# Kernel optimization log

Hardware: AMD Instinct MI355X
Metric: run time of the kernel (lower is better)

## Reference

```python
import jax, jax.numpy as jnp
import numpy as np

A = -0.75  # torch bicubic cubic-convolution coefficient

def _cubic_k(t):
    at = jnp.abs(t)
    return jnp.where(at <= 1, (A + 2) * at**3 - (A + 3) * at**2 + 1,
           jnp.where(at < 2, A * at**3 - 5 * A * at**2 + 8 * A * at - 4 * A, 0.0))

def _resize_last(x, out_size):
    # bicubic, align_corners=True, along last axis
    in_size = x.shape[-1]
    pos = jnp.arange(out_size, dtype=x.dtype) * ((in_size - 1) / (out_size - 1))
    i0 = jnp.floor(pos).astype(jnp.int32)
    frac = pos - i0
    offs = jnp.arange(-1, 3, dtype=jnp.int32)                    # 4 taps
    idx = jnp.clip(i0[None] + offs[:, None], 0, in_size - 1)     # [4, out]
    w = _cubic_k(frac[None] - offs[:, None].astype(x.dtype))     # [4, out]
    g = x[..., idx]                                              # [..., 4, out]
    return jnp.einsum('...ko,ko->...o', g, w)

def bicubic(x, H, W):
    x = _resize_last(x, W)
    x = jnp.swapaxes(_resize_last(jnp.swapaxes(x, -1, -2), H), -1, -2)
    return x

def conv(x, w, b):
    y = jax.lax.conv_general_dilated(x, w, (1, 1), 'SAME',
                                     dimension_numbers=('NCHW', 'OIHW', 'NCHW'))
    return y + b[None, :, None, None]

def pool(x):
    return jax.lax.reduce_window(x, -jnp.inf, jax.lax.max, (1, 1, 2, 2), (1, 1, 2, 2), 'VALID')

def extract(x, ws, bs):
    # feat1: vgg19 features[:2]
    x1 = jax.nn.relu(conv(x, ws[0], bs[0]))
    # feat2: vgg19 features[2:18]
    h = jax.nn.relu(conv(x1, ws[1], bs[1])); h = pool(h)
    h = jax.nn.relu(conv(h, ws[2], bs[2]))
    h = jax.nn.relu(conv(h, ws[3], bs[3])); h = pool(h)
    for i in range(4, 8):
        h = jax.nn.relu(conv(h, ws[i], bs[i]))
    h = bicubic(h, x1.shape[-2], x1.shape[-1])
    return jnp.concatenate([x1, h], axis=1)  # [B, 320, H, W]

def normalizer(f1, f2):
    B, C = f1.shape[:2]
    a = f1.reshape(B, C, -1)
    b = f2.reshape(B, C, -1)
    xc = jnp.concatenate([a, b], axis=-1)
    mean = xc.mean(-1, keepdims=True)
    std = xc.mean(-1, keepdims=True)  # faithful to original source bug: std = mean
    a = (a - mean) / (std + 1e-8)
    b = (b - mean) / (std + 1e-8)
    return a.reshape(f1.shape), b.reshape(f2.shape)

_CHANS = [(3, 64), (64, 64), (64, 128), (128, 128), (128, 256), (256, 256), (256, 256), (256, 256)]

def setup_inputs() -> dict:
    key = jax.random.key(0)
    ks = jax.random.split(key, 20)
    inp = {}
    for i, (ci, co) in enumerate(_CHANS):
        inp[f'w{i}'] = jax.random.normal(ks[i], (co, ci, 3, 3), jnp.float32) * np.sqrt(2.0 / (ci * 9))
        inp[f'b{i}'] = jnp.zeros((co,), jnp.float32)
    inp['x_ref'] = jax.random.normal(ks[16], (2, 3, 96, 96), jnp.float32)
    inp['x_template'] = jax.random.normal(ks[17], (2, 3, 48, 48), jnp.float32)
    inp['coef_ref'] = jnp.float32(1.0)
    inp['coef_tmp'] = jnp.float32(1.0)
    return inp

def reference(x_ref, x_template, coef_ref, coef_tmp,
              w0, b0, w1, b1, w2, b2, w3, b3, w4, b4, w5, b5, w6, b6, w7, b7):
    ws = [w0, w1, w2, w3, w4, w5, w6, w7]
    bs = [b0, b1, b2, b3, b4, b5, b6, b7]
    fref = extract(x_ref, ws, bs)
    ftem = extract(x_template, ws, bs)
    fref, ftem = normalizer(fref, ftem)
    B, C, m, n = fref.shape
    _, _, p, q = ftem.shape
    dist = jnp.einsum('bcmn,bcpq->bmnpq', fref, ftem).reshape(B, m * n, p * q)
    conf_ref = jax.nn.softmax(coef_ref * dist, axis=-2)
    conf_tmp = jax.nn.softmax(coef_tmp * dist, axis=-1)
    confidence = jnp.sqrt(conf_ref * conf_tmp)
    vals, _ = jax.lax.top_k(confidence, 10)
    values = vals.mean(-1, keepdims=True).reshape(B, m, n, 1)
    return values
```

## Files before the change

### kernel.cpp

```cpp
#include <hip/hip_runtime.h>
#include <math.h>

#define CK_A (-0.75f)

typedef __attribute__((ext_vector_type(8))) short bf16x8;
typedef __attribute__((ext_vector_type(4))) float f32x4;

struct CImg { const void* in; void* out; int H, W, tiles; long inBS, outBS, sStride; };

__device__ __forceinline__ float cubicw(float t){
  float at = fabsf(t);
  float at2 = at*at, at3 = at2*at;
  if (at <= 1.f) return (CK_A+2.f)*at3 - (CK_A+3.f)*at2 + 1.f;
  if (at < 2.f)  return CK_A*at3 - 5.f*CK_A*at2 + 8.f*CK_A*at - 4.f*CK_A;
  return 0.f;
}

__device__ __forceinline__ unsigned short f2bf_rne(float f){
  unsigned int u = __float_as_uint(f);
  unsigned int r = (u + 0x7fffu + ((u>>16)&1u)) >> 16;
  return (unsigned short)r;
}
__device__ __forceinline__ float bf2f(unsigned short h){
  return __uint_as_float(((unsigned int)h)<<16);
}
__device__ __forceinline__ unsigned pack_bf(float v){
  unsigned short h = f2bf_rne(v);
  unsigned short l = f2bf_rne(v - bf2f(h));
  return ((unsigned)h<<16) | (unsigned)l;
}
__device__ __forceinline__ float unpack_bf(unsigned p){
  return bf2f((unsigned short)(p>>16)) + bf2f((unsigned short)(p&0xffffu));
}

__device__ __forceinline__ void merge_ms(float& m, float& s, float m2, float s2){
  float M = fmaxf(m, m2);
  s = s*__expf(m - M) + s2*__expf(m2 - M);
  m = M;
}

#define MFB(a,b,c) __builtin_amdgcn_mfma_f32_16x16x32_bf16(a,b,c,0,0,0)

typedef const __attribute__((address_space(1))) unsigned int* gp1_t;
typedef __attribute__((address_space(3))) unsigned int* lp3_t;
__device__ __forceinline__ void dma16(const void* g, void* l){
  __builtin_amdgcn_global_load_lds((gp1_t)g, (lp3_t)l, 16, 0, 0);
}

__global__ __launch_bounds__(256) void conv0_d(CImg A, CImg B,
    const float* __restrict__ w, const float* __restrict__ bias,
    unsigned* __restrict__ pOutA, unsigned* __restrict__ pOutB){
  bool isA = (int)blockIdx.x < A.tiles;
  const float* in = (const float*)(isA ? A.in : B.in);
  float* out = (float*)(isA ? A.out : B.out);
  unsigned* pout = isA ? pOutA : pOutB;
  int H = isA ? A.H : B.H, W = isA ? A.W : B.W;
  long inBS = isA ? A.inBS : B.inBS, outBS = isA ? A.outBS : B.outBS;
  int tile = isA ? blockIdx.x : blockIdx.x - A.tiles;
  int tilesX = (W + 15) >> 4;
  int tx0 = (tile % tilesX) << 4, ty0 = (tile / tilesX) << 4;
  int cob = blockIdx.y * 4;
  int b = blockIdx.z;
  int lx = threadIdx.x & 15, ly = threadIdx.x >> 4;
  __shared__ float tile_s[3][18][20];
  float acc[4] = {0.f,0.f,0.f,0.f};
  const float* inb = in + (long)b*inBS;
  int ox = tx0+lx, oy = ty0+ly;
  int HW = H*W;

  for (int idx = threadIdx.x; idx < 3*324; idx += 256){
    int cl = idx/324, rem = idx - cl*324;
    int r = rem/18, c = rem - r*18;
    int gy = ty0 + r - 1, gx = tx0 + c - 1;
    const float* ic = inb + (long)cl*HW;
    tile_s[cl][r][c] = (gy>=0 && gy<H && gx>=0 && gx<W) ? ic[(long)gy*W+gx] : 0.f;
  }
  __syncthreads();
  #pragma unroll
  for (int cl=0; cl<3; cl++){
    float t00=tile_s[cl][ly+0][lx+0], t01=tile_s[cl][ly+0][lx+1], t02=tile_s[cl][ly+0][lx+2];
    float t10=tile_s[cl][ly+1][lx+0], t11=tile_s[cl][ly+1][lx+1], t12=tile_s[cl][ly+1][lx+2];
    float t20=tile_s[cl][ly+2][lx+0], t21=tile_s[cl][ly+2][lx+1], t22=tile_s[cl][ly+2][lx+2];
    #pragma unroll
    for (int j=0;j<4;j++){
      const float* wp = w + ((long)(cob+j)*3 + cl)*9;
      float a = acc[j];
      a = fmaf(t00, wp[0], a); a = fmaf(t01, wp[1], a); a = fmaf(t02, wp[2], a);
      a = fmaf(t10, wp[3], a); a = fmaf(t11, wp[4], a); a = fmaf(t12, wp[5], a);
      a = fmaf(t20, wp[6], a); a = fmaf(t21, wp[7], a); a = fmaf(t22, wp[8], a);
      acc[j] = a;
    }
  }
  if (ox < W && oy < H){
    #pragma unroll
    for (int j=0;j<4;j++){
      float v = fmaxf(acc[j] + bias[cob+j], 0.f);
      long pix = (long)(cob+j)*HW + (long)oy*W + ox;
      out[(long)b*outBS + pix] = v;
      pout[(long)b*64*HW + pix] = pack_bf(v);
    }
  }
}

__global__ void prep_w_all(const float* __restrict__ w1, const float* __restrict__ w2,
                           const float* __restrict__ w3, const float* __restrict__ w4,
                           const float* __restrict__ w5, const float* __restrict__ w6,
                           const float* __restrict__ w7, unsigned short* __restrict__ wp){
  const int ciT[7] = {64,64,128,128,256,256,256};
  const int coT[7] = {64,128,128,256,256,256,256};
  int l = blockIdx.y;
  const float* w = l==0?w1: l==1?w2: l==2?w3: l==3?w4: l==4?w5: l==5?w6: w7;
  long offv = 0;
  for (int i=0;i<7;i++){ if (i<l) offv += 9L*ciT[i]*coT[i]*2; }
  long total = 9L*ciT[l]*coT[l]*2;
  long e = (long)blockIdx.x*256 + threadIdx.x;
  if (e >= total) return;
  int CI = ciT[l], CO = coT[l];
  int j = (int)(e & 7);
  int lane = (int)((e>>3) & 63);
  int h = (int)((e>>9) & 1);
  long rem = e >> 10;
  int G = CO >> 4, KC = CI >> 5;
  int g = (int)(rem % G); long q = rem / G;
  int kc = (int)(q % KC); int o = (int)(q / KC);
  int co = (g<<4) + (lane & 15);
  int ci = (kc<<5) + ((lane>>4)<<3) + j;
  float v = w[((long)co*CI + ci)*9 + o];
  unsigned short hi = f2bf_rne(v);
  wp[offv + e] = (h==0) ? hi : f2bf_rne(v - bf2f(hi));
}

union AB { bf16x8 v; uint4 u; };

__global__ __launch_bounds__(256) void conv_mfma_d(
    CImg A, CImg B, const unsigned short* __restrict__ Wp,
    const float* __restrict__ bias, int CI, int CO, int nci, int S)
{
  bool isA = (int)blockIdx.x < A.tiles;
  const unsigned* in = (const unsigned*)(isA ? A.in : B.in);
  void* outv = isA ? A.out : B.out;
  int H = isA ? A.H : B.H, W = isA ? A.W : B.W;
  long inBS = isA ? A.inBS : B.inBS, outBS = isA ? A.outBS : B.outBS;
  long sStride = isA ? A.sStride : B.sStride;
  int tile = isA ? blockIdx.x : blockIdx.x - A.tiles;

  int HW = H*W;
  int tilesX = (W+7)>>3;
  int tx0 = (tile % tilesX)<<3, ty0 = (tile / tilesX)<<3;
  int cobase = blockIdx.y << 6;
  int s = blockIdx.z % S, b = blockIdx.z / S;
  int tid = threadIdx.x, lane = tid & 63, wid = tid>>6;
  int wm = wid>>1, wn = wid&1;
  int KC = CI>>5, G = CO>>4;
  __shared__ __align__(16) unsigned short Bth[4000];
  __shared__ __align__(16) unsigned short Btl[4000];
  const unsigned* inb = in + (long)b*inBS;

  int sofs[13]; int sla[13];
  #pragma unroll
  for (int i=0;i<13;i++){
    int e = tid + i*256;
    int cidx = e / 100, pix = e - cidx*100;
    int hy = pix/10, hx = pix - hy*10;
    int gy = ty0 - 1 + hy, gx = tx0 - 1 + hx;
    bool v = (gy>=0) && (gy<H) && (gx>=0) && (gx<W);
    sofs[i] = v ? (cidx*HW + gy*W + gx) : -1;
    sla[i] = pix*40 + cidx;
  }

  int n15 = lane & 15;
  int klane8 = (lane>>4)<<3;
  int p0 = wn*32 + n15;
  int base0 = ((p0>>3)*10 + (p0&7))*40 + klane8;
  int p1 = p0 + 16;
  int base1 = ((p1>>3)*10 + (p1&7))*40 + klane8;
  int g0 = (cobase>>4) + wm*2;

  f32x4 acc[2][2];
  #pragma unroll
  for (int i=0;i<2;i++)
    #pragma unroll
    for (int j=0;j<2;j++) acc[i][j] = (f32x4){0.f,0.f,0.f,0.f};

  int nkc = nci >> 5;
  for (int kk=0; kk<nkc; kk++){
    int ci0 = s*nci + (kk<<5);
    __syncthreads();
    #pragma unroll
    for (int i=0;i<12;i++){
      unsigned p = (sofs[i] >= 0) ? inb[(long)ci0*HW + sofs[i]] : 0u;
      Bth[sla[i]] = (unsigned short)(p>>16);
      Btl[sla[i]] = (unsigned short)(p & 0xffffu);
    }
    if (tid < 128){
      unsigned p = (sofs[12] >= 0) ? inb[(long)ci0*HW + sofs[12]] : 0u;
      Bth[sla[12]] = (unsigned short)(p>>16);
      Btl[sla[12]] = (unsigned short)(p & 0xffffu);
    }
    __syncthreads();
    int kc = ci0 >> 5;
    const unsigned short* wpb = Wp + (long)kc*G*1024 + (long)lane*8;
    #pragma unroll
    for (int o=0;o<9;o++){
      const int dy = o/3, dx = o - dy*3;
      const int sh = (dy*10+dx)*40;
      const unsigned short* wo = wpb + (long)o*KC*G*1024;
      AB a0h,a0l,a1h,a1l, b0h,b0l,b1h,b1l;
      a0h.u = *(const uint4*)(wo + (long)g0*1024);
      a0l.u = *(const uint4*)(wo + (long)g0*1024 + 512);
      a1h.u = *(const uint4*)(wo + (long)(g0+1)*1024);
      a1l.u = *(const uint4*)(wo + (long)(g0+1)*1024 + 512);
      b0h.v = *(const bf16x8*)&Bth[base0 + sh];
      b0l.v = *(const bf16x8*)&Btl[base0 + sh];
      b1h.v = *(const bf16x8*)&Bth[base1 + sh];
      b1l.v = *(const bf16x8*)&Btl[base1 + sh];
      acc[0][0] = MFB(a0h.v, b0l.v, acc[0][0]);
      acc[0][0] = MFB(a0l.v, b0h.v, acc[0][0]);
      acc[0][0] = MFB(a0h.v, b0h.v, acc[0][0]);
      acc[0][1] = MFB(a0h.v, b1l.v, acc[0][1]);
      acc[0][1] = MFB(a0l.v, b1h.v, acc[0][1]);
      acc[0][1] = MFB(a0h.v, b1h.v, acc[0][1]);
      acc[1][0] = MFB(a1h.v, b0l.v, acc[1][0]);
      acc[1][0] = MFB(a1l.v, b0h.v, acc[1][0]);
      acc[1][0] = MFB(a1h.v, b0h.v, acc[1][0]);
      acc[1][1] = MFB(a1h.v, b1l.v, acc[1][1]);
      acc[1][1] = MFB(a1l.v, b1h.v, acc[1][1]);
      acc[1][1] = MFB(a1h.v, b1h.v, acc[1][1]);
    }
  }

  #pragma unroll
  for (int ng=0; ng<2; ng++){
    int p = wn*32 + ng*16 + n15;
    int gy = ty0 + (p>>3), gx = tx0 + (p&7);
    bool ok = (gy<H) && (gx<W);
    #pragma unroll
    for (int mg=0; mg<2; mg++){
      #pragma unroll
      for (int r=0;r<4;r++){
        if (ok){
          int co = cobase + wm*32 + mg*16 + ((lane>>4)<<2) + r;
          long idx = (long)co*HW + (long)gy*W + gx;
          float v = acc[mg][ng][r];
          if (bias){
            unsigned* outp = (unsigned*)outv + (long)b*outBS;
            outp[idx] = pack_bf(fmaxf(v + bias[co], 0.f));
          } else {
            float* outp = (float*)outv + (long)s*sStride + (long)b*outBS;
            outp[idx] = v;
          }
        }
      }
    }
  }
}

__global__ void reduce_d(const float* __restrict__ pA, const float* __restrict__ pB,
                         const float* __restrict__ bias,
                         unsigned* __restrict__ oA, unsigned* __restrict__ oB,
                         int S, long sStrA, long sStrB, int CO, int HWa, int HWb,
                         long oBSa, long oBSb){
  int img = blockIdx.y;
  const float* part = img ? pB : pA;
  unsigned* out = img ? oB : oA;
  int HW = img ? HWb : HWa;
  long sStride = img ? sStrB : sStrA;
  long outBS = img ? oBSb : oBSa;
  long tot = 2L*CO*HW;
  long e = (long)blockIdx.x*256 + threadIdx.x;
  if (e >= tot) return;
  long b = e / ((long)CO*HW);
  long r = e - b*(long)CO*HW;
  float v = 0.f;
  for (int s=0;s<S;s++) v += part[(long)s*sStride + e];
  int co = (int)(r / HW);
  out[b*outBS + r] = pack_bf(fmaxf(v + bias[co], 0.f));
}

__global__ void maxpool2_d(const unsigned* __restrict__ inA, unsigned* __restrict__ outA, long NCa, int HiA, int WiA,
                           const unsigned* __restrict__ inB, unsigned* __restrict__ outB, long NCb, int HiB, int WiB){
  const unsigned* in = blockIdx.y ? inB : inA;
  unsigned* out = blockIdx.y ? outB : outA;
  long NC = blockIdx.y ? NCb : NCa;
  int Hi = blockIdx.y ? HiB : HiA, Wi = blockIdx.y ? WiB : WiA;
  int Ho = Hi>>1, Wo = Wi>>1;
  long total = NC * Ho * Wo;
  long idx = (long)blockIdx.x*256 + threadIdx.x;
  if (idx >= total) return;
  int x = (int)(idx % Wo); long t = idx / Wo; int y = (int)(t % Ho); long nc = t / Ho;
  const unsigned* p = in + (nc*Hi + 2*y)*(long)Wi + 2*x;
  unsigned c0=p[0], c1=p[1], c2=p[Wi], c3=p[Wi+1];
  float v0=unpack_bf(c0), v1=unpack_bf(c1), v2=unpack_bf(c2), v3=unpack_bf(c3);
  unsigned best=c0; float bv=v0;
  if (v1>bv){bv=v1;best=c1;}
  if (v2>bv){bv=v2;best=c2;}
  if (v3>bv){bv=v3;best=c3;}
  out[idx] = best;
}

__global__ __launch_bounds__(256) void bicubic_d(
    const unsigned* __restrict__ inA, float* __restrict__ outA,
    const unsigned* __restrict__ inB, float* __restrict__ outB){
  int c = blockIdx.x;
  int img = blockIdx.y >> 1, b = blockIdx.y & 1;
  const unsigned* in = img ? inB : inA;
  float* out = img ? outB : outA;
  int Hin = img ? 12 : 24, Win = Hin, Hout = img ? 48 : 96, Wout = Hout;
  long inBS = img ? 256L*144 : 256L*576;
  long outBS = img ? 320L*2304 : 320L*9216;
  __shared__ float s[576];
  const unsigned* ip = in + (long)b*inBS + (long)c*Hin*Win;
  float* op = out + (long)b*outBS + (long)c*Hout*Wout;
  int n = Hin*Win;
  for (int i = threadIdx.x; i < n; i += 256) s[i] = unpack_bf(ip[i]);
  __syncthreads();
  float scy = (float)((double)(Hin-1)/(double)(Hout-1));
  float scx = scy;
  int total = Hout*Wout;
  for (int idx = threadIdx.x; idx < total; idx += 256){
    int ox = idx % Wout, oy = idx / Wout;
    float py = oy * scy, px = ox * scx;
    float iy0f = floorf(py), ix0f = floorf(px);
    int iy0 = (int)iy0f, ix0 = (int)ix0f;
    float fy = py - iy0f, fx = px - ix0f;
    float wy[4], wx[4]; int xs[4], ys[4];
    #pragma unroll
    for (int t=0;t<4;t++){
      wy[t] = cubicw(fy - (float)(t-1));
      wx[t] = cubicw(fx - (float)(t-1));
      ys[t] = min(max(iy0 + t - 1, 0), Hin-1);
      xs[t] = min(max(ix0 + t - 1, 0), Win-1);
    }
    float acc = 0.f;
    #pragma unroll
    for (int i=0;i<4;i++){
      const float* row = &s[ys[i]*Win];
      float rs = wx[0]*row[xs[0]] + wx[1]*row[xs[1]] + wx[2]*row[xs[2]] + wx[3]*row[xs[3]];
      acc = fmaf(wy[i], rs, acc);
    }
    op[idx] = acc;
  }
}

__global__ __launch_bounds__(256) void mean_k(const float* __restrict__ fR, const float* __restrict__ fT, float* __restrict__ mean){
  int c = blockIdx.x % 320, b = blockIdx.x / 320;
  const float* a = fR + ((long)b*320+c)*9216L;
  const float* t = fT + ((long)b*320+c)*2304L;
  float s = 0.f;
  for (int i=threadIdx.x;i<9216;i+=256) s += a[i];
  for (int i=threadIdx.x;i<2304;i+=256) s += t[i];
  __shared__ float sm[4];
  for (int o=32;o;o>>=1) s += __shfl_down(s,o);
  int lane = threadIdx.x & 63, wv = threadIdx.x >> 6;
  if (lane==0) sm[wv] = s;
  __syncthreads();
  if (threadIdx.x==0) mean[b*320+c] = (sm[0]+sm[1]+sm[2]+sm[3]) * (1.f/11520.f);
}

__global__ __launch_bounds__(256) void split_bf16_d(const float* __restrict__ fR, const float* __restrict__ fT,
    const float* __restrict__ mean,
    unsigned short* __restrict__ AhR, unsigned short* __restrict__ AlR,
    unsigned short* __restrict__ BhT, unsigned short* __restrict__ BlT){
  bool isR = blockIdx.x < 288;
  const float* feat = isR ? fR : fT;
  unsigned short* oh = isR ? AhR : BhT;
  unsigned short* ol = isR ? AlR : BlT;
  int P = isR ? 9216 : 2304;
  int m0 = (isR ? blockIdx.x : blockIdx.x - 288) * 32;
  int b = blockIdx.y;
  __shared__ unsigned int t[32][321];
  int ml = threadIdx.x & 31, kq = threadIdx.x >> 5;
  const float* fp = feat + (long)b*320*P + m0 + ml;
  for (int k = kq*40; k < kq*40+40; k++){
    float mu = mean[b*320+k];
    float v = (fp[(long)k*P] - mu) / (mu + 1e-8f);
    t[ml][k] = pack_bf(v);
  }
  __syncthreads();
  long base = ((long)b*P + m0)*320;
  for (int idx = threadIdx.x; idx < 32*320; idx += 256){
    int m = idx/320, k = idx - m*320;
    unsigned int p = t[m][k];
    oh[base + (long)m*320 + k] = (unsigned short)(p>>16);
    ol[base + (long)m*320 + k] = (unsigned short)(p & 0xffffu);
  }
}

__global__ __launch_bounds__(256) void gemm_mfma(
    const unsigned short* __restrict__ Ah, const unsigned short* __restrict__ Al,
    const unsigned short* __restrict__ Bh, const unsigned short* __restrict__ Bl,
    float* __restrict__ D, const float* __restrict__ coefr,
    float* __restrict__ pm, float* __restrict__ ps){
  const int N = 2304, K = 320;
  int flat = (int)blockIdx.y * 18 + (int)blockIdx.x;
  int nf = (flat & 7) * 162 + (flat >> 3);
  int mb = nf / 18, nb = nf - mb*18;
  int n0 = nb*128, m0 = mb*128;
  __shared__ __align__(16) unsigned short SF[16384];
  int tid = threadIdx.x, lane = tid & 63, wid = tid >> 6;
  int wm = wid >> 1, wn = wid & 1;
  int n15 = lane & 15, q = lane >> 4;
  f32x4 acc[4][4];
  #pragma unroll
  for (int i=0;i<4;i++)
    #pragma unroll
    for (int j=0;j<4;j++) acc[i][j] = (f32x4){0.f,0.f,0.f,0.f};

  const unsigned short* srcB[8];
  #pragma unroll
  for (int i=0;i<8;i++){
    int li = i*256 + tid;
    int rem = li & 1023;
    int row = rem >> 3, sg = rem & 7;
    int seg = sg ^ (row & 7);
    if (li < 1024) srcB[i] = ((seg<4) ? Ah : Al) + (long)(m0+row)*K + (seg&3)*8;
    else           srcB[i] = ((seg<4) ? Bh : Bl) + (long)(n0+row)*K + (seg&3)*8;
  }

  int aH[4], aL[4], bH[4], bL[4];
  #pragma unroll
  for (int g=0; g<4; g++){
    int ra = wm*64 + g*16 + n15;
    int rb = wn*64 + g*16 + n15;
    aH[g] = ra*64 + (( q   ) ^ (ra&7))*8;
    aL[g] = ra*64 + ((q+4) ^ (ra&7))*8;
    bH[g] = 8192 + rb*64 + (( q   ) ^ (rb&7))*8;
    bL[g] = 8192 + rb*64 + ((q+4) ^ (rb&7))*8;
  }

  for (int k0=0; k0<K; k0+=32){
    __syncthreads();
    #pragma unroll
    for (int i=0;i<8;i++){
      dma16(srcB[i] + k0, (void*)&SF[((i<<8) + (wid<<6))<<3]);
    }
    __syncthreads();

    AB af[2][4], bf[2][4];
    #pragma unroll
    for (int g=0; g<4; g++){
      af[0][g].v = *(const bf16x8*)&SF[aH[g]];
      af[1][g].v = *(const bf16x8*)&SF[aL[g]];
      bf[0][g].v = *(const bf16x8*)&SF[bH[g]];
      bf[1][g].v = *(const bf16x8*)&SF[bL[g]];
    }
    #pragma unroll
    for (int mg=0; mg<4; mg++)
      #pragma unroll
      for (int ng=0; ng<4; ng++){
        acc[mg][ng] = MFB(af[0][mg].v, bf[1][ng].v, acc[mg][ng]);
        acc[mg][ng] = MFB(af[1][mg].v, bf[0][ng].v, acc[mg][ng]);
        acc[mg][ng] = MFB(af[0][mg].v, bf[0][ng].v, acc[mg][ng]);
      }
  }
  __syncthreads();

  #pragma unroll
  for (int mg=0; mg<4; mg++)
    #pragma unroll
    for (int ng=0; ng<4; ng++){
      int col = n0 + wn*64 + ng*16 + n15;
      #pragma unroll
      for (int r=0;r<4;r++){
        int rowv = m0 + wm*64 + mg*16 + q*4 + r;
        __builtin_nontemporal_store(acc[mg][ng][r], &D[(long)rowv*N + col]);
      }
    }

  float cr = *coefr;
  float* red = (float*)&SF[0];
  float pmv[4], psv[4];
  #pragma unroll
  for (int ng=0; ng<4; ng++){
    float m = -INFINITY;
    #pragma unroll
    for (int mg=0; mg<4; mg++)
      #pragma unroll
      for (int r=0;r<4;r++) m = fmaxf(m, cr*acc[mg][ng][r]);
    float s = 0.f;
    #pragma unroll
    for (int mg=0; mg<4; mg++)
      #pragma unroll
      for (int r=0;r<4;r++) s += __expf(cr*acc[mg][ng][r] - m);
    #pragma unroll
    for (int o=16;o<64;o<<=1){
      float m2 = __shfl_xor(m,o), s2 = __shfl_xor(s,o);
      merge_ms(m,s,m2,s2);
    }
    pmv[ng]=m; psv[ng]=s;
  }
  if (q==0){
    #pragma unroll
    for (int ng=0; ng<4; ng++){
      int cl = wn*64 + ng*16 + lane;
      red[wm*128 + cl] = pmv[ng];
      red[256 + wm*128 + cl] = psv[ng];
    }
  }
  __syncthreads();
  if (wm==0 && q==0){
    #pragma unroll
    for (int ng=0; ng<4; ng++){
      int cl = wn*64 + ng*16 + lane;
      float m = pmv[ng], s = psv[ng];
      merge_ms(m, s, red[128+cl], red[384+cl]);
      pm[(long)mb*2304 + n0 + cl] = m;
      ps[(long)mb*2304 + n0 + cl] = s;
    }
  }
}

__global__ void colstat_merge(const float* __restrict__ pm, const float* __restrict__ ps,
                              float* __restrict__ qcol){
  int idx = blockIdx.x*256 + threadIdx.x;
  if (idx >= 2304) return;
  float m=-INFINITY, s=0.f;
  for (int k=0;k<72;k++) merge_ms(m, s, pm[(long)k*2304+idx], ps[(long)k*2304+idx]);
  qcol[idx] = 0.5f*m + 0.5f*__logf(s);
}

__global__ __launch_bounds__(256) void conf_topk_f(const float* __restrict__ D,
    const float* __restrict__ coefr, const float* __restrict__ coeft,
    const float* __restrict__ qcol, float* __restrict__ outp){
  int m = blockIdx.x;
  const float* drow = D + (long)m*2304;
  int tid = threadIdx.x, lane = tid & 63, wv = tid >> 6;
  float ct = *coeft, cr = *coefr;
  float v[9], tv[9];
  #pragma unroll
  for (int i=0;i<9;i++){ v[i] = __builtin_nontemporal_load(&drow[tid + i*256]); tv[i] = ct * v[i]; }

  __shared__ float sred[8];
  __shared__ unsigned int cand[40];

  float mx = tv[0];
  #pragma unroll
  for (int i=1;i<9;i++) mx = fmaxf(mx, tv[i]);
  #pragma unroll
  for (int o=1;o<64;o<<=1) mx = fmaxf(mx, __shfl_xor(mx, o));
  if (lane==0) sred[wv] = mx;
  __syncthreads();
  mx = fmaxf(fmaxf(sred[0],sred[1]), fmaxf(sred[2],sred[3]));
  float s = 0.f;
  #pragma unroll
  for (int i=0;i<9;i++) s += __expf(tv[i]-mx);
  #pragma unroll
  for (int o=1;o<64;o<<=1) s += __shfl_xor(s, o);
  if (lane==0) sred[4+wv] = s;
  __syncthreads();
  float rs = sred[4]+sred[5]+sred[6]+sred[7];
  float rho = 0.5f*mx + 0.5f*__logf(rs);
  float hc = 0.5f*(cr+ct);

  unsigned int key[9];
  #pragma unroll
  for (int i=0;i<9;i++){
    int n = i*256 + tid;
    float t = fmaf(hc, v[i], -qcol[n]);
    unsigned int b = __float_as_uint(t);
    b ^= (b >> 31) ? 0xFFFFFFFFu : 0x80000000u;
    key[i] = (b & 0xFFFFF000u) | (unsigned)n;
  }

  for (int t10=0; t10<10; t10++){
    unsigned int lb = key[0];
    #pragma unroll
    for (int i=1;i<9;i++) lb = lb > key[i] ? lb : key[i];
    unsigned int wb = lb;
    #pragma unroll
    for (int o=1;o<64;o<<=1){
      unsigned int x = (unsigned int)__shfl_xor((int)wb, o);
      wb = wb > x ? wb : x;
    }
    if (lane==0) cand[wv*10 + t10] = wb;
    #pragma unroll
    for (int i=0;i<9;i++) if (key[i]==wb) key[i]=0;
  }
  __syncthreads();

  if (wv == 0){
    unsigned int k = (lane < 40) ? cand[lane] : 0u;
    int sel = -1;
    for (int t10=0; t10<10; t10++){
      unsigned int wb = k;
      #pragma unroll
      for (int o=1;o<64;o<<=1){
        unsigned int x = (unsigned int)__shfl_xor((int)wb, o);
        wb = wb > x ? wb : x;
      }
      if (k == wb) k = 0;
      if (lane == t10) sel = (int)(wb & 0xFFFu);
    }
    float c = 0.f;
    if (sel >= 0){
      float t = fmaf(hc, drow[sel], -qcol[sel]);
      c = __expf(t - rho);
    }
    #pragma unroll
    for (int o=1;o<64;o<<=1) c += __shfl_xor(c, o);
    if (lane == 0) outp[m] = c * 0.1f;
  }
}

extern "C" void kernel_launch(void* const* d_in, const int* in_sizes, int n_in,
                              void* d_out, int out_size, void* d_ws, size_t ws_size,
                              hipStream_t stream) {
  const float *W[8], *Bp[8], *xr, *xt, *cr, *ct;
  if (in_sizes[0] == 1728){
    for (int i=0;i<8;i++){ W[i]=(const float*)d_in[2*i]; Bp[i]=(const float*)d_in[2*i+1]; }
    xr=(const float*)d_in[16]; xt=(const float*)d_in[17];
    cr=(const float*)d_in[18]; ct=(const float*)d_in[19];
  } else {
    xr=(const float*)d_in[0]; xt=(const float*)d_in[1];
    cr=(const float*)d_in[2]; ct=(const float*)d_in[3];
    for (int i=0;i<8;i++){ W[i]=(const float*)d_in[4+2*i]; Bp[i]=(const float*)d_in[5+2*i]; }
  }

  const int convCI[8] = {3,64,64,128,128,256,256,256};
  const int convCO[8] = {64,64,128,128,256,256,256,256};
  long wpoff[8]; long wtot = 0;
  for (int l=1;l<8;l++){ wpoff[l] = wtot; wtot += 9L*convCI[l]*convCO[l]*2; }

  float* ws = (float*)d_ws;
  long off = 0;
  auto alloc = [&](long nfl){ float* p = ws + off; off += (nfl + 63) & ~63L; return p; };
  float* featR = alloc(2L*320*9216);
  float* featT = alloc(2L*320*2304);
  float* meanb = alloc(640);
  float* pm    = alloc(72L*2304);
  float* ps    = alloc(72L*2304);
  float* qcol  = alloc(2304);
  unsigned short* wp = (unsigned short*)alloc((wtot+1)/2);
  float* scratch = alloc(9216L*2304);
  if ((size_t)(off*4) > ws_size) return;

  unsigned short* AhR = (unsigned short*)alloc((2L*9216*320 + 1)/2);
  unsigned short* AlR = (unsigned short*)alloc((2L*9216*320 + 1)/2);
  unsigned short* BhT = (unsigned short*)alloc((2L*2304*320 + 1)/2);
  unsigned short* BlT = (unsigned short*)alloc((2L*2304*320 + 1)/2);
  if ((size_t)(off*4) > ws_size) return;

  unsigned* pc0R = (unsigned*)scratch;
  unsigned* pc0T = pc0R + 1179648;
  unsigned* rA   = pc0T + 294912;
  unsigned* rB   = rA + 1179648;
  unsigned* rC   = rB + 294912;
  unsigned* rD   = rC + 589824;
  unsigned* rE   = rD + 589824;
  unsigned* rF   = rE + 147456;
  unsigned* rG   = rF + 294912;
  unsigned* a2   = rG + 294912;
  unsigned* b2   = a2 + 294912;
  unsigned* c2   = b2 + 73728;
  unsigned* d2   = c2 + 147456;
  unsigned* e2   = d2 + 147456;
  unsigned* f2   = e2 + 36864;
  unsigned* g2   = f2 + 73728;
  float* tPR = (float*)(g2 + 73728);
  float* tPT = tPR + 1179648;
  float* dist = scratch;

  auto mkimg = [](const void* in, void* out, int H, int Wd, int tiles,
                  long inBS, long outBS, long sStr){
    CImg c; c.in=in; c.out=out; c.H=H; c.W=Wd; c.tiles=tiles;
    c.inBS=inBS; c.outBS=outBS; c.sStride=sStr; return c;
  };

  prep_w_all<<<dim3(4608,7), 256, 0, stream>>>(W[1],W[2],W[3],W[4],W[5],W[6],W[7], wp);

  {
    CImg A = mkimg(xr, featR, 96,96, 36, 3L*9216, 320L*9216, 0);
    CImg B = mkimg(xt, featT, 48,48, 9, 3L*2304, 320L*2304, 0);
    conv0_d<<<dim3(45,16,2), 256, 0, stream>>>(A, B, W[0], Bp[0], pc0R, pc0T);
  }
  {
    CImg A = mkimg(pc0R, rA, 96,96, 144, 64L*9216, 64L*9216, 0);
    CImg B = mkimg(pc0T, a2, 48,48, 36, 64L*2304, 64L*2304, 0);
    conv_mfma_d<<<dim3(180,1,2), 256, 0, stream>>>(A,B, wp+wpoff[1], Bp[1], 64,64,64,1);
  }
  maxpool2_d<<<dim3(1152,2), 256, 0, stream>>>(rA,rB,128,96,96, a2,b2,128,48,48);
  {
    CImg A = mkimg(rB, tPR, 48,48, 36, 64L*2304, 128L*2304, 589824);
    CImg B = mkimg(b2, tPT, 24,24, 9, 64L*576, 128L*576, 147456);
    conv_mfma_d<<<dim3(45,2,4), 256, 0, stream>>>(A,B, wp+wpoff[2], nullptr, 64,128,32,2);
    reduce_d<<<dim3(2304,2), 256, 0, stream>>>(tPR,tPT,Bp[2], rC,c2, 2, 589824,147456, 128, 2304,576, 128L*2304, 128L*576);
  }
  {
    CImg A = mkimg(rC, tPR, 48,48, 36, 128L*2304, 128L*2304, 589824);
    CImg B = mkimg(c2, tPT, 24,24, 9, 128L*576, 128L*576, 147456);
    conv_mfma_d<<<dim3(45,2,4), 256, 0, stream>>>(A,B, wp+wpoff[3], nullptr, 128,128,64,2);
    reduce_d<<<dim3(2304,2), 256, 0, stream>>>(tPR,tPT,Bp[3], rD,d2, 2, 589824,147456, 128, 2304,576, 128L*2304, 128L*576);
  }
  maxpool2_d<<<dim3(576,2), 256, 0, stream>>>(rD,rE,256,48,48, d2,e2,256,24,24);
  {
    CImg A = mkimg(rE, tPR, 24,24, 9, 128L*576, 256L*576, 294912);
    CImg B = mkimg(e2, tPT, 12,12, 4, 128L*144, 256L*144, 73728);
    conv_mfma_d<<<dim3(13,4,8), 256, 0, stream>>>(A,B, wp+wpoff[4], nullptr, 128,256,32,4);
    reduce_d<<<dim3(1152,2), 256, 0, stream>>>(tPR,tPT,Bp[4], rF,f2, 4, 294912,73728, 256, 576,144, 256L*576, 256L*144);
  }
  const unsigned* inR[3] = {rF, rG, rF};  unsigned* outR[3] = {rG, rF, rG};
  const unsigned* inT[3] = {f2, g2, f2};  unsigned* outT[3] = {g2, f2, g2};
  for (int i=0;i<3;i++){
    int l = 5+i;
    CImg A = mkimg(inR[i], tPR, 24,24, 9, 256L*576, 256L*576, 294912);
    CImg B = mkimg(inT[i], tPT, 12,12, 4, 256L*144, 256L*144, 73728);
    conv_mfma_d<<<dim3(13,4,8), 256, 0, stream>>>(A,B, wp+wpoff[l], nullptr, 256,256,64,4);
    reduce_d<<<dim3(1152,2), 256, 0, stream>>>(tPR,tPT,Bp[l], outR[i],outT[i], 4, 294912,73728, 256, 576,144, 256L*576, 256L*144);
  }
  bicubic_d<<<dim3(256,4), 256, 0, stream>>>(rG, featR + 64L*9216, g2, featT + 64L*2304);

  mean_k<<<640, 256, 0, stream>>>(featR, featT, meanb);
  split_bf16_d<<<dim3(360,2), 256, 0, stream>>>(featR, featT, meanb, AhR, AlR, BhT, BlT);

  for (int b=0; b<2; b++){
    gemm_mfma<<<dim3(18,72), 256, 0, stream>>>(
        AhR + (long)b*9216*320, AlR + (long)b*9216*320,
        BhT + (long)b*2304*320, BlT + (long)b*2304*320, dist, cr, pm, ps);
    colstat_merge<<<dim3(9), 256, 0, stream>>>(pm, ps, qcol);
    conf_topk_f<<<dim3(9216), 256, 0, stream>>>(dist, cr, ct, qcol, (float*)d_out + (long)b*9216);
  }
}
```

Baseline: 452.3 us.

## Fuse maxpool into conv epilogues and fold channel-mean into producers

The first 2x2 maxpool moves into the epilogue of the layer-1 MFMA conv, which stages ReLU outputs in shared memory and writes pooled bf16 directly. The second pool is fused into the split-K reduction kernel (reduce_pool_d). The separate mean_k pass is removed: per-channel sums are now accumulated with atomics in conv0 and bicubic, with the 1/11520 scaling applied in split_bf16. This cuts several full-feature-map round trips and kernel launches, at the cost of a memset, atomics and a different floating-point summation order.

After: 490.1 us. 8.4% more time.

```diff
diff --git a/kernel.cpp b/kernel.cpp
--- a/kernel.cpp
+++ b/kernel.cpp
@@ -49,7 +49,8 @@
 
 __global__ __launch_bounds__(256) void conv0_d(CImg A, CImg B,
     const float* __restrict__ w, const float* __restrict__ bias,
-    unsigned* __restrict__ pOutA, unsigned* __restrict__ pOutB){
+    unsigned* __restrict__ pOutA, unsigned* __restrict__ pOutB,
+    float* __restrict__ meanb){
   bool isA = (int)blockIdx.x < A.tiles;
   const float* in = (const float*)(isA ? A.in : B.in);
   float* out = (float*)(isA ? A.out : B.out);
@@ -63,6 +64,7 @@
   int b = blockIdx.z;
   int lx = threadIdx.x & 15, ly = threadIdx.x >> 4;
   __shared__ float tile_s[3][18][20];
+  __shared__ float credu[4][4];
   float acc[4] = {0.f,0.f,0.f,0.f};
   const float* inb = in + (long)b*inBS;
   int ox = tx0+lx, oy = ty0+ly;
@@ -91,14 +93,27 @@
       acc[j] = a;
     }
   }
-  if (ox < W && oy < H){
-    #pragma unroll
-    for (int j=0;j<4;j++){
-      float v = fmaxf(acc[j] + bias[cob+j], 0.f);
-      long pix = (long)(cob+j)*HW + (long)oy*W + ox;
-      out[(long)b*outBS + pix] = v;
-      pout[(long)b*64*HW + pix] = pack_bf(v);
-    }
+  int lane = threadIdx.x & 63, wv = threadIdx.x >> 6;
+  #pragma unroll
+  for (int j=0;j<4;j++){
+    float v = fmaxf(acc[j] + bias[cob+j], 0.f);
+    long pix = (long)(cob+j)*HW + (long)oy*W + ox;
+    out[(long)b*outBS + pix] = v;
+    pout[(long)b*64*HW + pix] = pack_bf(v);
+    acc[j] = v;
+  }
+  #pragma unroll
+  for (int j=0;j<4;j++){
+    float s = acc[j];
+    #pragma unroll
+    for (int o=1;o<64;o<<=1) s += __shfl_xor(s, o);
+    if (lane==0) credu[j][wv] = s;
+  }
+  __syncthreads();
+  if (threadIdx.x < 4){
+    int j = threadIdx.x;
+    float s = credu[j][0]+credu[j][1]+credu[j][2]+credu[j][3];
+    atomicAdd(&meanb[b*320 + cob + j], s);
   }
 }
 
@@ -134,11 +149,14 @@
 
 __global__ __launch_bounds__(256) void conv_mfma_d(
     CImg A, CImg B, const unsigned short* __restrict__ Wp,
-    const float* __restrict__ bias, int CI, int CO, int nci, int S)
+    const float* __restrict__ bias, int CI, int CO, int nci, int S,
+    unsigned* __restrict__ poolA, unsigned* __restrict__ poolB, long poolBSa, long poolBSb)
 {
   bool isA = (int)blockIdx.x < A.tiles;
   const unsigned* in = (const unsigned*)(isA ? A.in : B.in);
   void* outv = isA ? A.out : B.out;
+  unsigned* poolOut = isA ? poolA : poolB;
+  long poolBS = isA ? poolBSa : poolBSb;
   int H = isA ? A.H : B.H, W = isA ? A.W : B.W;
   long inBS = isA ? A.inBS : B.inBS, outBS = isA ? A.outBS : B.outBS;
   long sStride = isA ? A.sStride : B.sStride;
@@ -152,8 +170,9 @@
   int tid = threadIdx.x, lane = tid & 63, wid = tid>>6;
   int wm = wid>>1, wn = wid&1;
   int KC = CI>>5, G = CO>>4;
-  __shared__ __align__(16) unsigned short Bth[4000];
-  __shared__ __align__(16) unsigned short Btl[4000];
+  __shared__ __align__(16) char smem[16928];
+  unsigned short* Bth = (unsigned short*)smem;
+  unsigned short* Btl = Bth + 4000;
   const unsigned* inb = in + (long)b*inBS;
 
   int sofs[13]; int sla[13];
@@ -229,6 +248,39 @@
     }
   }
 
+  if (poolOut){
+    float* pbuf = (float*)smem;
+    __syncthreads();
+    #pragma unroll
+    for (int ng=0; ng<2; ng++){
+      int p = wn*32 + ng*16 + n15;
+      #pragma unroll
+      for (int mg=0; mg<2; mg++){
+        #pragma unroll
+        for (int r=0;r<4;r++){
+          int col = wm*32 + mg*16 + ((lane>>4)<<2) + r;
+          float v = fmaxf(acc[mg][ng][r] + bias[cobase + col], 0.f);
+          pbuf[col*66 + p] = v;
+        }
+      }
+    }
+    __syncthreads();
+    int Wp2 = W>>1, HWp = (H>>1)*Wp2;
+    unsigned* outp = poolOut + (long)b*poolBS;
+    #pragma unroll
+    for (int t=0;t<4;t++){
+      int o = tid*4 + t;
+      int col = o >> 4, pp = o & 15;
+      int py = pp >> 2, px2 = pp & 3;
+      int pbase = col*66 + py*16 + px2*2;
+      float v0 = pbuf[pbase], v1 = pbuf[pbase+1];
+      float v2 = pbuf[pbase+8], v3 = pbuf[pbase+9];
+      float mx = fmaxf(fmaxf(v0,v1), fmaxf(v2,v3));
+      outp[(long)(cobase+col)*HWp + (long)((ty0>>1)+py)*Wp2 + (tx0>>1)+px2] = pack_bf(mx);
+    }
+    return;
+  }
+
   #pragma unroll
   for (int ng=0; ng<2; ng++){
     int p = wn*32 + ng*16 + n15;
@@ -277,30 +329,40 @@
   out[b*outBS + r] = pack_bf(fmaxf(v + bias[co], 0.f));
 }
 
-__global__ void maxpool2_d(const unsigned* __restrict__ inA, unsigned* __restrict__ outA, long NCa, int HiA, int WiA,
-                           const unsigned* __restrict__ inB, unsigned* __restrict__ outB, long NCb, int HiB, int WiB){
-  const unsigned* in = blockIdx.y ? inB : inA;
-  unsigned* out = blockIdx.y ? outB : outA;
-  long NC = blockIdx.y ? NCb : NCa;
-  int Hi = blockIdx.y ? HiB : HiA, Wi = blockIdx.y ? WiB : WiA;
-  int Ho = Hi>>1, Wo = Wi>>1;
-  long total = NC * Ho * Wo;
-  long idx = (long)blockIdx.x*256 + threadIdx.x;
-  if (idx >= total) return;
-  int x = (int)(idx % Wo); long t = idx / Wo; int y = (int)(t % Ho); long nc = t / Ho;
-  const unsigned* p = in + (nc*Hi + 2*y)*(long)Wi + 2*x;
-  unsigned c0=p[0], c1=p[1], c2=p[Wi], c3=p[Wi+1];
-  float v0=unpack_bf(c0), v1=unpack_bf(c1), v2=unpack_bf(c2), v3=unpack_bf(c3);
-  unsigned best=c0; float bv=v0;
-  if (v1>bv){bv=v1;best=c1;}
-  if (v2>bv){bv=v2;best=c2;}
-  if (v3>bv){bv=v3;best=c3;}
-  out[idx] = best;
+__global__ void reduce_pool_d(const float* __restrict__ pA, const float* __restrict__ pB,
+                              const float* __restrict__ bias,
+                              unsigned* __restrict__ oA, unsigned* __restrict__ oB,
+                              int S, long sStrA, long sStrB, int CO, int Ha, int Wa,
+                              int Hb, int Wb){
+  int img = blockIdx.y;
+  const float* part = img ? pB : pA;
+  unsigned* out = img ? oB : oA;
+  int H = img ? Hb : Ha, W = img ? Wb : Wa;
+  long sStride = img ? sStrB : sStrA;
+  int Hp = H>>1, Wp = W>>1;
+  long tot = 2L*CO*Hp*Wp;
+  long e = (long)blockIdx.x*256 + threadIdx.x;
+  if (e >= tot) return;
+  int x = (int)(e % Wp); long t = e / Wp;
+  int y = (int)(t % Hp); t /= Hp;
+  int ch = (int)(t % CO); long b = t / CO;
+  float bI = bias[ch];
+  long base = b*(long)CO*H*W + (long)ch*H*W + (long)(2*y)*W + 2*x;
+  long po[4] = {base, base+1, base+W, base+W+1};
+  float mx = -INFINITY;
+  #pragma unroll
+  for (int k=0;k<4;k++){
+    float a = bI;
+    for (int s=0;s<S;s++) a += part[(long)s*sStride + po[k]];
+    mx = fmaxf(mx, fmaxf(a, 0.f));
+  }
+  out[e] = pack_bf(mx);
 }
 
 __global__ __launch_bounds__(256) void bicubic_d(
     const unsigned* __restrict__ inA, float* __restrict__ outA,
-    const unsigned* __restrict__ inB, float* __restrict__ outB){
+    const unsigned* __restrict__ inB, float* __restrict__ outB,
+    float* __restrict__ meanb){
   int c = blockIdx.x;
   int img = blockIdx.y >> 1, b = blockIdx.y & 1;
   const unsigned* in = img ? inB : inA;
@@ -309,6 +371,7 @@
   long inBS = img ? 256L*144 : 256L*576;
   long outBS = img ? 320L*2304 : 320L*9216;
   __shared__ float s[576];
+  __shared__ float sred[4];
   const unsigned* ip = in + (long)b*inBS + (long)c*Hin*Win;
   float* op = out + (long)b*outBS + (long)c*Hout*Wout;
   int n = Hin*Win;
@@ -317,6 +380,7 @@
   float scy = (float)((double)(Hin-1)/(double)(Hout-1));
   float scx = scy;
   int total = Hout*Wout;
+  float lsum = 0.f;
   for (int idx = threadIdx.x; idx < total; idx += 256){
     int ox = idx % Wout, oy = idx / Wout;
     float py = oy * scy, px = ox * scx;
@@ -339,22 +403,15 @@
       acc = fmaf(wy[i], rs, acc);
     }
     op[idx] = acc;
-  }
-}
-
-__global__ __launch_bounds__(256) void mean_k(const float* __restrict__ fR, const float* __restrict__ fT, float* __restrict__ mean){
-  int c = blockIdx.x % 320, b = blockIdx.x / 320;
-  const float* a = fR + ((long)b*320+c)*9216L;
-  const float* t = fT + ((long)b*320+c)*2304L;
-  float s = 0.f;
-  for (int i=threadIdx.x;i<9216;i+=256) s += a[i];
-  for (int i=threadIdx.x;i<2304;i+=256) s += t[i];
-  __shared__ float sm[4];
-  for (int o=32;o;o>>=1) s += __shfl_down(s,o);
+    lsum += acc;
+  }
   int lane = threadIdx.x & 63, wv = threadIdx.x >> 6;
-  if (lane==0) sm[wv] = s;
-  __syncthreads();
-  if (threadIdx.x==0) mean[b*320+c] = (sm[0]+sm[1]+sm[2]+sm[3]) * (1.f/11520.f);
+  #pragma unroll
+  for (int o=1;o<64;o<<=1) lsum += __shfl_xor(lsum, o);
+  if (lane==0) sred[wv] = lsum;
+  __syncthreads();
+  if (threadIdx.x==0)
+    atomicAdd(&meanb[b*320 + 64 + c], sred[0]+sred[1]+sred[2]+sred[3]);
 }
 
 __global__ __launch_bounds__(256) void split_bf16_d(const float* __restrict__ fR, const float* __restrict__ fT,
@@ -372,7 +429,7 @@
   int ml = threadIdx.x & 31, kq = threadIdx.x >> 5;
   const float* fp = feat + (long)b*320*P + m0 + ml;
   for (int k = kq*40; k < kq*40+40; k++){
-    float mu = mean[b*320+k];
+    float mu = mean[b*320+k] * (1.f/11520.f);
     float v = (fp[(long)k*P] - mu) / (mu + 1e-8f);
     t[ml][k] = pack_bf(v);
   }
@@ -642,19 +699,15 @@
 
   unsigned* pc0R = (unsigned*)scratch;
   unsigned* pc0T = pc0R + 1179648;
-  unsigned* rA   = pc0T + 294912;
-  unsigned* rB   = rA + 1179648;
-  unsigned* rC   = rB + 294912;
-  unsigned* rD   = rC + 589824;
-  unsigned* rE   = rD + 589824;
-  unsigned* rF   = rE + 147456;
+  unsigned* rB   = pc0T + 294912;
+  unsigned* b2   = rB + 294912;
+  unsigned* rC   = b2 + 73728;
+  unsigned* c2   = rC + 589824;
+  unsigned* rE   = c2 + 147456;
+  unsigned* e2   = rE + 147456;
+  unsigned* rF   = e2 + 36864;
   unsigned* rG   = rF + 294912;
-  unsigned* a2   = rG + 294912;
-  unsigned* b2   = a2 + 294912;
-  unsigned* c2   = b2 + 73728;
-  unsigned* d2   = c2 + 147456;
-  unsigned* e2   = d2 + 147456;
-  unsigned* f2   = e2 + 36864;
+  unsigned* f2   = rG + 294912;
   unsigned* g2   = f2 + 73728;
   float* tPR = (float*)(g2 + 73728);
   float* tPT = tPR + 1179648;
@@ -666,36 +719,40 @@
     c.inBS=inBS; c.outBS=outBS; c.sStride=sStr; return c;
   };
 
+  hipMemsetAsync(meanb, 0, 640*sizeof(float), stream);
   prep_w_all<<<dim3(4608,7), 256, 0, stream>>>(W[1],W[2],W[3],W[4],W[5],W[6],W[7], wp);
 
   {
     CImg A = mkimg(xr, featR, 96,96, 36, 3L*9216, 320L*9216, 0);
     CImg B = mkimg(xt, featT, 48,48, 9, 3L*2304, 320L*2304, 0);
-    conv0_d<<<dim3(45,16,2), 256, 0, stream>>>(A, B, W[0], Bp[0], pc0R, pc0T);
+    conv0_d<<<dim3(45,16,2), 256, 0, stream>>>(A, B, W[0], Bp[0], pc0R, pc0T, meanb);
   }
   {
-    CImg A = mkimg(pc0R, rA, 96,96, 144, 64L*9216, 64L*9216, 0);
-    CImg B = mkimg(pc0T, a2, 48,48, 36, 64L*2304, 64L*2304, 0);
-    conv_mfma_d<<<dim3(180,1,2), 256, 0, stream>>>(A,B, wp+wpoff[1], Bp[1], 64,64,64,1);
-  }
-  maxpool2_d<<<dim3(1152,2), 256, 0, stream>>>(rA,rB,128,96,96, a2,b2,128,48,48);
+    CImg A = mkimg(pc0R, nullptr, 96,96, 144, 64L*9216, 0, 0);
+    CImg B = mkimg(pc0T, nullptr, 48,48, 36, 64L*2304, 0, 0);
+    conv_mfma_d<<<dim3(180,1,2), 256, 0, stream>>>(A,B, wp+wpoff[1], Bp[1], 64,64,64,1,
+                                                   rB, b2, 64L*2304, 64L*576);
+  }
   {
     CImg A = mkimg(rB, tPR, 48,48, 36, 64L*2304, 128L*2304, 589824);
     CImg B = mkimg(b2, tPT, 24,24, 9, 64L*576, 128L*576, 147456);
-    conv_mfma_d<<<dim3(45,2,4), 256, 0, stream>>>(A,B, wp+wpoff[2], nullptr, 64,128,32,2);
+    conv_mfma_d<<<dim3(45,2,4), 256, 0, stream>>>(A,B, wp+wpoff[2], nullptr, 64,128,32,2,
+                                                  nullptr,nullptr,0,0);
     reduce_d<<<dim3(2304,2), 256, 0, stream>>>(tPR,tPT,Bp[2], rC,c2, 2, 589824,147456, 128, 2304,576, 128L*2304, 128L*576);
   }
   {
     CImg A = mkimg(rC, tPR, 48,48, 36, 128L*2304, 128L*2304, 589824);
     CImg B = mkimg(c2, tPT, 24,24, 9, 128L*576, 128L*576, 147456);
-    conv_mfma_d<<<dim3(45,2,4), 256, 0, stream>>>(A,B, wp+wpoff[3], nullptr, 128,128,64,2);
-    reduce_d<<<dim3(2304,2), 256, 0, stream>>>(tPR,tPT,Bp[3], rD,d2, 2, 589824,147456, 128, 2304,576, 128L*2304, 128L*576);
-  }
-  maxpool2_d<<<dim3(576,2), 256, 0, stream>>>(rD,rE,256,48,48, d2,e2,256,24,24);
+    conv_mfma_d<<<dim3(45,2,4), 256, 0, stream>>>(A,B, wp+wpoff[3], nullptr, 128,128,64,2,
+                                                  nullptr,nullptr,0,0);
+    reduce_pool_d<<<dim3(576,2), 256, 0, stream>>>(tPR,tPT,Bp[3], rE,e2, 2, 589824,147456,
+                                                   128, 48,48, 24,24);
+  }
   {
     CImg A = mkimg(rE, tPR, 24,24, 9, 128L*576, 256L*576, 294912);
     CImg B = mkimg(e2, tPT, 12,12, 4, 128L*144, 256L*144, 73728);
-    conv_mfma_d<<<dim3(13,4,8), 256, 0, stream>>>(A,B, wp+wpoff[4], nullptr, 128,256,32,4);
+    conv_mfma_d<<<dim3(13,4,8), 256, 0, stream>>>(A,B, wp+wpoff[4], nullptr, 128,256,32,4,
+                                                  nullptr,nullptr,0,0);
     reduce_d<<<dim3(1152,2), 256, 0, stream>>>(tPR,tPT,Bp[4], rF,f2, 4, 294912,73728, 256, 576,144, 256L*576, 256L*144);
   }
   const unsigned* inR[3] = {rF, rG, rF};  unsigned* outR[3] = {rG, rF, rG};
@@ -704,12 +761,12 @@
     int l = 5+i;
     CImg A = mkimg(inR[i], tPR, 24,24, 9, 256L*576, 256L*576, 294912);
     CImg B = mkimg(inT[i], tPT, 12,12, 4, 256L*144, 256L*144, 73728);
-    conv_mfma_d<<<dim3(13,4,8), 256, 0, stream>>>(A,B, wp+wpoff[l], nullptr, 256,256,64,4);
+    conv_mfma_d<<<dim3(13,4,8), 256, 0, stream>>>(A,B, wp+wpoff[l], nullptr, 256,256,64,4,
+                                                  nullptr,nullptr,0,0);
     reduce_d<<<dim3(1152,2), 256, 0, stream>>>(tPR,tPT,Bp[l], outR[i],outT[i], 4, 294912,73728, 256, 576,144, 256L*576, 256L*144);
   }
-  bicubic_d<<<dim3(256,4), 256, 0, stream>>>(rG, featR + 64L*9216, g2, featT + 64L*2304);
-
-  mean_k<<<640, 256, 0, stream>>>(featR, featT, meanb);
+  bicubic_d<<<dim3(256,4), 256, 0, stream>>>(rG, featR + 64L*9216, g2, featT + 64L*2304, meanb);
+
   split_bf16_d<<<dim3(360,2), 256, 0, stream>>>(featR, featT, meanb, AhR, AlR, BhT, BlT);
 
   for (int b=0; b<2; b++){
```
